# Optimization experiments

Measured on AMD Instinct MI355X. Metric: run time of the kernel, lower is better.

Reference implementation:

```python
import jax, jax.numpy as jnp
import numpy as np

B, S, HID = 2, 2048, 2048
NH, HD = 16, 128
EPS = 1e-5
ROPE_BASE = 10000.0


def setup_inputs() -> dict:
    key = jax.random.key(0)
    k1, k2, k3 = jax.random.split(key, 3)
    std = 1.0 / np.sqrt(HID)
    x = jax.random.normal(k1, (B, S, HID), jnp.float32)
    w_in = jax.random.truncated_normal(k2, -3.0, 3.0, (3 * NH * HD, HID), jnp.float32) * std
    std_o = std / np.sqrt(2.0)  # layer_id = 0 -> std / sqrt(2*(0+1))
    w_out = jax.random.truncated_normal(k3, -3.0, 3.0, (HID, NH * HD), jnp.float32) * std_o
    q_norm_w = jnp.ones((NH * HD,), jnp.float32)
    k_norm_w = jnp.ones((NH * HD,), jnp.float32)
    return {"x": x, "w_in": w_in, "w_out": w_out, "q_norm_w": q_norm_w, "k_norm_w": k_norm_w}


def _rms_norm(x, w, eps=EPS):
    ms = jnp.mean(x * x, axis=-1, keepdims=True)
    return x * jax.lax.rsqrt(ms + eps) * w


def _rope(x, offset=0):
    # x: [B, S, NH, HD]; rotate-half convention
    half = HD // 2
    inv_freq = 1.0 / (ROPE_BASE ** (jnp.arange(half, dtype=jnp.float32) / half))
    pos = jnp.arange(x.shape[1], dtype=jnp.float32) + offset
    ang = pos[:, None] * inv_freq                      # [S, half]
    cos = jnp.cos(ang)[None, :, None, :]
    sin = jnp.sin(ang)[None, :, None, :]
    x1, x2 = jnp.split(x, 2, axis=-1)
    return jnp.concatenate([x1 * cos - x2 * sin, x2 * cos + x1 * sin], axis=-1)


def reference(x, w_in, w_out, q_norm_w, k_norm_w):
    b, s, _ = x.shape
    qkv = jnp.einsum('bsh,oh->bso', x, w_in)           # [B, S, 3*NH*HD]
    q, k, v = jnp.split(qkv, 3, axis=-1)
    # qk-norm over the flat (NH*HD) axis, as in the torch module
    q = _rms_norm(q, q_norm_w)
    k = _rms_norm(k, k_norm_w)
    q = q.reshape(b, s, NH, HD)
    k = k.reshape(b, s, NH, HD)
    v = v.reshape(b, s, NH, HD)
    q = _rope(q)
    k = _rope(k)
    scale = 1.0 / np.sqrt(HD)
    scores = jnp.einsum('bqhd,bkhd->bhqk', q, k) * scale
    causal = jnp.tril(jnp.ones((s, s), dtype=bool))
    scores = jnp.where(causal[None, None, :, :], scores, jnp.finfo(scores.dtype).min)
    probs = jax.nn.softmax(scores, axis=-1)
    out = jnp.einsum('bhqk,bkhd->bqhd', probs, v).reshape(b, s, NH * HD)
    return jnp.einsum('bso,ho->bsh', out, w_out)
```

## Files before the change

### kernel.cpp

```cpp
#include <hip/hip_runtime.h>
#include <hip/hip_bf16.h>
#include <math.h>

#define B_   2
#define S_   2048
#define HID_ 2048
#define NH_  16
#define HD_  128
#define QKV_ (3 * NH_ * HD_)
#define EPS_ 1e-5f

typedef __bf16 bf16x8 __attribute__((ext_vector_type(8)));
typedef __bf16 bf16x4 __attribute__((ext_vector_type(4)));
typedef __bf16 bf16x2 __attribute__((ext_vector_type(2)));
typedef float  f32x4  __attribute__((ext_vector_type(4)));

__global__ __launch_bounds__(256) void cast3_f32_bf16(
    const float* __restrict__ a, __bf16* __restrict__ ao, int na4,
    const float* __restrict__ b, __bf16* __restrict__ bo, int nb4,
    const float* __restrict__ c, __bf16* __restrict__ co, int nc4) {
    int j = blockIdx.x * 256 + threadIdx.x;
    const float* src;
    __bf16* dst;
    if (j < na4) {
        src = a; dst = ao;
    } else {
        j -= na4;
        if (j < nb4) {
            src = b; dst = bo;
        } else {
            j -= nb4;
            if (j >= nc4) return;
            src = c; dst = co;
        }
    }
    float4 v = reinterpret_cast<const float4*>(src)[j];
    bf16x4 o = {(__bf16)v.x, (__bf16)v.y, (__bf16)v.z, (__bf16)v.w};
    reinterpret_cast<bf16x4*>(dst)[j] = o;
}

__device__ __forceinline__ void gload_lds16(const __bf16* g, __bf16* l) {
    __builtin_amdgcn_global_load_lds(
        (const __attribute__((address_space(1))) void*)g,
        (__attribute__((address_space(3))) void*)l, 16, 0, 0);
}

#define BARR  __builtin_amdgcn_s_barrier()
#define LGKM0 asm volatile("s_waitcnt lgkmcnt(0)" ::: "memory")
#define FENCE asm volatile("" ::: "memory")

__device__ __forceinline__ void read_a4x(const __bf16* bc, int wm, int lrow,
                                         int quad, int swz, int qq,
                                         bf16x8 (&af)[2][2]) {
#pragma unroll
    for (int i2 = 0; i2 < 2; ++i2)
#pragma unroll
        for (int kk = 0; kk < 2; ++kk)
            af[i2][kk] = *reinterpret_cast<const bf16x8*>(
                &bc[(wm * 128 + (qq * 2 + i2) * 16 + lrow) * 64 +
                    (((kk * 4 + quad) ^ swz) << 3)]);
}

__device__ __forceinline__ void read_b6(const __bf16* bc, int wn, int lrow,
                                        int quad, int swz,
                                        bf16x8 (&bf)[3][2]) {
#pragma unroll
    for (int j = 0; j < 3; ++j)
#pragma unroll
        for (int kk = 0; kk < 2; ++kk)
            bf[j][kk] = *reinterpret_cast<const bf16x8*>(
                &bc[16384 + (wn * 48 + j * 16 + lrow) * 64 +
                    (((kk * 4 + quad) ^ swz) << 3)]);
}

__device__ __forceinline__ void mfma12(int qq, const bf16x8 (&af)[2][2],
                                       const bf16x8 (&bf)[3][2],
                                       f32x4 (&acc)[8][3]) {
    __builtin_amdgcn_s_setprio(1);
#pragma unroll
    for (int i2 = 0; i2 < 2; ++i2)
#pragma unroll
        for (int j = 0; j < 3; ++j)
#pragma unroll
            for (int kk = 0; kk < 2; ++kk)
                acc[qq * 2 + i2][j] = __builtin_amdgcn_mfma_f32_16x16x32_bf16(
                    af[i2][kk], bf[j][kk], acc[qq * 2 + i2][j], 0, 0, 0);
    __builtin_amdgcn_s_setprio(0);
}

__global__ __launch_bounds__(512, 2) void gemm1_192(
    const __bf16* __restrict__ A, const __bf16* __restrict__ Bm,
    __bf16* __restrict__ C, int M, int N, int K) {
    __shared__ __bf16 lds[2][28672];

    const int tid  = threadIdx.x;
    const int w    = tid >> 6;
    const int lane = tid & 63;
    const int lrow = lane & 15;
    const int quad = lane >> 4;
    const int wm   = w >> 2;
    const int wn   = w & 3;
    const int swz  = lrow & 7;

    const int chunk = (int)gridDim.x >> 3;
    const int flat  = (int)blockIdx.x;
    const int vid   = (flat & 7) * chunk + (flat >> 3);
    const int m0 = (vid & 15) * 256;
    const int n0 = (vid >> 4) * 192;

    const int lr = lane >> 3;
    const int lg = lane & 7;
    const size_t K64 = (size_t)K * 64;
    const __bf16* pA = A  + (size_t)(m0 + w * 8 + lr) * K + ((lg ^ lr) << 3);
    const __bf16* pB = Bm + (size_t)(n0 + w * 8 + lr) * K + ((lg ^ lr) << 3);

#define STA(c, tt, dst) gload_lds16(pA + (size_t)(c) * K64 + (size_t)(tt) * 64, \
                                    (dst) + (c) * 4096 + w * 512)
#define STB(c, tt, dst) gload_lds16(pB + (size_t)(c) * K64 + (size_t)(tt) * 64, \
                                    (dst) + 16384 + (c) * 4096 + w * 512)

    f32x4 acc[8][3] = {};
    bf16x8 af[2][2], bf[3][2];

    {
        __bf16* d = &lds[0][0];
        STB(0, 0, d); STB(1, 0, d); STB(2, 0, d);
        FENCE;
        STA(0, 0, d); STA(2, 0, d);
        FENCE;
        STA(1, 0, d); STA(3, 0, d);
    }
    asm volatile("s_waitcnt vmcnt(2)" ::: "memory");
    BARR;

    const int nt = K >> 6;
    for (int t = 0; t < nt - 1; ++t) {
        __bf16* bc = &lds[t & 1][0];
        __bf16* bn = &lds[(t & 1) ^ 1][0];
        const int tn = t + 1;
        read_a4x(bc, wm, lrow, quad, swz, 0, af);
        read_b6(bc, wn, lrow, quad, swz, bf);
        STB(0, tn, bn); STB(1, tn, bn);
        BARR; LGKM0;
        mfma12(0, af, bf, acc);
        BARR;
        read_a4x(bc, wm, lrow, quad, swz, 1, af);
        STB(2, tn, bn);
        BARR; LGKM0;
        mfma12(1, af, bf, acc);
        asm volatile("s_waitcnt vmcnt(3)" ::: "memory");
        BARR;
        read_a4x(bc, wm, lrow, quad, swz, 2, af);
        STA(0, tn, bn); STA(2, tn, bn);
        BARR; LGKM0;
        mfma12(2, af, bf, acc);
        BARR;
        read_a4x(bc, wm, lrow, quad, swz, 3, af);
        STA(1, tn, bn); STA(3, tn, bn);
        BARR; LGKM0;
        mfma12(3, af, bf, acc);
        asm volatile("s_waitcnt vmcnt(2)" ::: "memory");
        BARR;
    }
    {
        __bf16* bc = &lds[(nt - 1) & 1][0];
        read_a4x(bc, wm, lrow, quad, swz, 0, af);
        read_b6(bc, wn, lrow, quad, swz, bf);
        BARR; LGKM0;
        mfma12(0, af, bf, acc);
        BARR;
        read_a4x(bc, wm, lrow, quad, swz, 1, af);
        BARR; LGKM0;
        mfma12(1, af, bf, acc);
        asm volatile("s_waitcnt vmcnt(0)" ::: "memory");
        BARR;
        read_a4x(bc, wm, lrow, quad, swz, 2, af);
        BARR; LGKM0;
        mfma12(2, af, bf, acc);
        BARR;
        read_a4x(bc, wm, lrow, quad, swz, 3, af);
        BARR; LGKM0;
        mfma12(3, af, bf, acc);
    }
#undef STA
#undef STB

#pragma unroll
    for (int mf = 0; mf < 8; ++mf) {
#pragma unroll
        for (int r = 0; r < 4; ++r) {
            int row = m0 + wm * 128 + mf * 16 + quad * 4 + r;
            size_t cb = (size_t)row * N + n0 + wn * 48 + lrow;
#pragma unroll
            for (int j = 0; j < 3; ++j)
                C[cb + j * 16] = (__bf16)acc[mf][j][r];
        }
    }
}

__device__ __forceinline__ void stage_tile6(
    const __bf16* pA, const __bf16* pB, __bf16* buf, int w, int K) {
#pragma unroll
    for (int s = 0; s < 2; ++s)
        gload_lds16(pA + (size_t)s * 64 * K, buf + s * 4096 + w * 512);
#pragma unroll
    for (int s = 0; s < 4; ++s)
        gload_lds16(pB + (size_t)s * 64 * K, buf + 8192 + s * 4096 + w * 512);
}

template <typename OutT>
__global__ __launch_bounds__(512, 2) void gemm_bt_8ph(
    const __bf16* __restrict__ A, const __bf16* __restrict__ Bm,
    OutT* __restrict__ C, int M, int N, int K) {
    __shared__ __bf16 lds[3][24576];

    const int tid  = threadIdx.x;
    const int w    = tid >> 6;
    const int lane = tid & 63;
    const int lrow = lane & 15;
    const int quad = lane >> 4;
    const int wm   = w >> 2;
    const int wn   = w & 3;

    const int chunk = (int)gridDim.x >> 3;
    const int flat  = (int)blockIdx.x;
    const int vid   = (flat & 7) * chunk + (flat >> 3);
    const int by    = vid & 31;
    const int bx    = vid >> 5;
    const int m0 = by * 128;
    const int n0 = bx * 256;

    const int lr = lane >> 3;
    const int lg = lane & 7;
    const __bf16* pA = A  + (size_t)(m0 + w * 8 + lr) * K + ((lg ^ lr) << 3);
    const __bf16* pB = Bm + (size_t)(n0 + w * 8 + lr) * K + ((lg ^ lr) << 3);

    const int nt = K >> 6;
    f32x4 acc[4][4] = {};

    stage_tile6(pA, pB, &lds[0][0], w, K);
    stage_tile6(pA + 64, pB + 64, &lds[1][0], w, K);

    int cur = 0;
    for (int t = 0; t < nt; ++t) {
        __bf16* bufc = &lds[cur][0];
        int nxt = cur + 2; if (nxt >= 3) nxt -= 3;
        if (t + 2 < nt) {
            stage_tile6(pA + (size_t)(t + 2) * 64, pB + (size_t)(t + 2) * 64,
                        &lds[nxt][0], w, K);
            asm volatile("s_waitcnt vmcnt(12)" ::: "memory");
        } else if (t + 1 < nt) {
            asm volatile("s_waitcnt vmcnt(6)" ::: "memory");
        } else {
            asm volatile("s_waitcnt vmcnt(0)" ::: "memory");
        }
        BARR;
        FENCE;

#pragma unroll
        for (int q = 0; q < 2; ++q) {
            bf16x8 af[2][2], bfv[4][2];
#pragma unroll
            for (int i = 0; i < 2; ++i)
#pragma unroll
                for (int kk = 0; kk < 2; ++kk)
                    af[i][kk] = *reinterpret_cast<const bf16x8*>(
                        &bufc[(wm * 64 + (q * 2 + i) * 16 + lrow) * 64 +
                              (((kk * 4 + quad) ^ (lrow & 7)) << 3)]);
#pragma unroll
            for (int j = 0; j < 4; ++j)
#pragma unroll
                for (int kk = 0; kk < 2; ++kk)
                    bfv[j][kk] = *reinterpret_cast<const bf16x8*>(
                        &bufc[8192 + (wn * 64 + j * 16 + lrow) * 64 +
                              (((kk * 4 + quad) ^ (lrow & 7)) << 3)]);
            BARR;
            FENCE;
            __builtin_amdgcn_s_setprio(1);
#pragma unroll
            for (int i = 0; i < 2; ++i)
#pragma unroll
                for (int j = 0; j < 4; ++j)
#pragma unroll
                    for (int kk = 0; kk < 2; ++kk)
                        acc[q * 2 + i][j] =
                            __builtin_amdgcn_mfma_f32_16x16x32_bf16(
                                af[i][kk], bfv[j][kk], acc[q * 2 + i][j],
                                0, 0, 0);
            __builtin_amdgcn_s_setprio(0);
        }
        BARR;
        FENCE;
        cur = (cur == 2) ? 0 : cur + 1;
    }

#pragma unroll
    for (int mi = 0; mi < 4; ++mi) {
#pragma unroll
        for (int r = 0; r < 4; ++r) {
            int row = m0 + wm * 64 + mi * 16 + quad * 4 + r;
            size_t basec = (size_t)row * N + n0 + wn * 64 + lrow;
#pragma unroll
            for (int nj = 0; nj < 4; ++nj)
                C[basec + nj * 16] = (OutT)acc[mi][nj][r];
        }
    }
}

__global__ __launch_bounds__(256) void normrope_kernel(
    __bf16* __restrict__ qkv, const float* __restrict__ qw,
    const float* __restrict__ kw) {
    const int row = blockIdx.x;
    const int sel = blockIdx.y;
    const int pos = row & (S_ - 1);
    __bf16* p = qkv + (size_t)row * QKV_ + sel * 2048;
    const float* w = sel ? kw : qw;

    __shared__ float buf[2048];
    __shared__ float red[4];
    const int tid = threadIdx.x;
    const int e   = tid * 8;

    bf16x8 t = *reinterpret_cast<const bf16x8*>(&p[e]);
    float xs[8];
    float ss = 0.f;
#pragma unroll
    for (int u = 0; u < 8; ++u) {
        xs[u] = (float)t[u];
        buf[e + u] = xs[u];
        ss += xs[u] * xs[u];
    }
#pragma unroll
    for (int off = 32; off > 0; off >>= 1) ss += __shfl_xor(ss, off, 64);
    if ((tid & 63) == 0) red[tid >> 6] = ss;
    __syncthreads();
    float total = red[0] + red[1] + red[2] + red[3];
    float scale = rsqrtf(total * (1.f / 2048.f) + EPS_);

    const float kfreq2 = -0.20762050593046f;
    const int jbase = e & 63;
    const bool first = (e & 127) < 64;
    const int ep = e ^ 64;

    float ps[8], ws[8], pw[8];
#pragma unroll
    for (int u = 0; u < 8; ++u) ps[u] = buf[ep + u];
    float4 w0 = *reinterpret_cast<const float4*>(&w[e]);
    float4 w1 = *reinterpret_cast<const float4*>(&w[e + 4]);
    float4 p0 = *reinterpret_cast<const float4*>(&w[ep]);
    float4 p1 = *reinterpret_cast<const float4*>(&w[ep + 4]);
    ws[0]=w0.x; ws[1]=w0.y; ws[2]=w0.z; ws[3]=w0.w;
    ws[4]=w1.x; ws[5]=w1.y; ws[6]=w1.z; ws[7]=w1.w;
    pw[0]=p0.x; pw[1]=p0.y; pw[2]=p0.z; pw[3]=p0.w;
    pw[4]=p1.x; pw[5]=p1.y; pw[6]=p1.z; pw[7]=p1.w;

    bf16x8 o8;
#pragma unroll
    for (int u = 0; u < 8; ++u) {
        float inv_freq = exp2f((float)(jbase + u) * kfreq2);
        float ang = (float)pos * inv_freq;
        float sn = __sinf(ang);
        float cs = __cosf(ang);
        float a  = xs[u] * scale * ws[u];
        float bb = ps[u] * scale * pw[u];
        float o  = first ? (a * cs - bb * sn) : (a * cs + bb * sn);
        o8[u] = (__bf16)o;
    }
    *reinterpret_cast<bf16x8*>(&p[e]) = o8;
}

#define VTP 36

__global__ __launch_bounds__(512, 4) void attn_mfma(
    const __bf16* __restrict__ qkv, __bf16* __restrict__ aout) {
    const int flat = (int)blockIdx.x;
    const int vid  = (flat & 7) * 64 + (flat >> 3);
    const int bh   = vid >> 4;
    const int qt   = 15 - (vid & 15);
    const int b    = bh >> 4;
    const int h    = bh & (NH_ - 1);
    const int q0   = qt * 128;
    const int tid  = threadIdx.x;
    const int w    = tid >> 6;
    const int lane = tid & 63;
    const int lrow = lane & 15;
    const int quad = lane >> 4;

    __shared__ __bf16 Ks[2][4][32 * 32];
    __shared__ __bf16 Vt[2][128 * VTP];
    __shared__ __bf16 Pb[8][16 * VTP];

    const size_t base = (size_t)(b * S_) * QKV_ + (size_t)h * HD_;
    const int qrow = q0 + w * 16 + lrow;

    bf16x8 qf[4];
#pragma unroll
    for (int kc = 0; kc < 4; ++kc)
        qf[kc] = *reinterpret_cast<const bf16x8*>(
            &qkv[base + (size_t)qrow * QKV_ + kc * 32 + quad * 8]);

    f32x4 o[8] = {};
    float lpart = 0.f;

    const int ktmax_w   = 4 * qt + (w >> 1);
    const int ktmax_blk = 4 * qt + 3;
    const float sl2 = 0.12751743671f;

    const __bf16* kg0 = qkv + base + 2048 +
                        (size_t)((w & 1) * 16 + (lane >> 2)) * QKV_ +
                        (w >> 1) * 32 + (lane & 3) * 8;
    const int g  = tid >> 4;
    const int kp = tid & 15;
    const __bf16* vg0 = qkv + base + 4096 + (size_t)(kp * 2) * QKV_ + g * 8;

    gload_lds16(kg0, &Ks[0][w >> 1][(w & 1) * 512]);
    bf16x8 v0 = {}, v1 = {};
    if (tid < 256) {
        v0 = *reinterpret_cast<const bf16x8*>(vg0);
        v1 = *reinterpret_cast<const bf16x8*>(vg0 + QKV_);
    }

    for (int kt = 0; kt <= ktmax_blk; ++kt) {
        const int buf = kt & 1;
        if (tid < 256) {
#pragma unroll
            for (int u = 0; u < 8; ++u) {
                bf16x2 pr = {v0[u], v1[u]};
                *reinterpret_cast<bf16x2*>(
                    &Vt[buf][(g * 8 + u) * VTP + kp * 2]) = pr;
            }
        }
        __syncthreads();
        if (kt < ktmax_blk) {
            const __bf16* kg = kg0 + (size_t)(kt + 1) * 32 * QKV_;
            gload_lds16(kg, &Ks[buf ^ 1][w >> 1][(w & 1) * 512]);
            if (tid < 256) {
                const __bf16* vg = vg0 + (size_t)(kt + 1) * 32 * QKV_;
                v0 = *reinterpret_cast<const bf16x8*>(vg);
                v1 = *reinterpret_cast<const bf16x8*>(vg + QKV_);
            }
        }
        if (kt <= ktmax_w) {
            f32x4 sc[2] = {};
            __builtin_amdgcn_s_setprio(1);
#pragma unroll
            for (int kc = 0; kc < 4; ++kc) {
                bf16x8 kf0 = *reinterpret_cast<const bf16x8*>(
                    &Ks[buf][kc][lrow * 32 + quad * 8]);
                bf16x8 kf1 = *reinterpret_cast<const bf16x8*>(
                    &Ks[buf][kc][(16 + lrow) * 32 + quad * 8]);
                sc[0] = __builtin_amdgcn_mfma_f32_16x16x32_bf16(
                    kf0, qf[kc], sc[0], 0, 0, 0);
                sc[1] = __builtin_amdgcn_mfma_f32_16x16x32_bf16(
                    kf1, qf[kc], sc[1], 0, 0, 0);
            }
            __builtin_amdgcn_s_setprio(0);
            const bool diag = (kt == ktmax_w);
            float p[2][4];
#pragma unroll
            for (int m2 = 0; m2 < 2; ++m2)
#pragma unroll
                for (int r = 0; r < 4; ++r) {
                    float s = sc[m2][r] * sl2 - 32.f;
                    if (diag && kt * 32 + m2 * 16 + quad * 4 + r > qrow)
                        s = -1e30f;
                    p[m2][r] = exp2f(s);
                    lpart += p[m2][r];
                }
#pragma unroll
            for (int m2 = 0; m2 < 2; ++m2) {
                bf16x4 pb = {(__bf16)p[m2][0], (__bf16)p[m2][1],
                             (__bf16)p[m2][2], (__bf16)p[m2][3]};
                *reinterpret_cast<bf16x4*>(
                    &Pb[w][lrow * VTP + m2 * 16 + quad * 4]) = pb;
            }
            bf16x8 pf = *reinterpret_cast<const bf16x8*>(
                &Pb[w][lrow * VTP + quad * 8]);
            __builtin_amdgcn_s_setprio(1);
#pragma unroll
            for (int dt = 0; dt < 8; ++dt) {
                bf16x8 vf = *reinterpret_cast<const bf16x8*>(
                    &Vt[buf][(dt * 16 + lrow) * VTP + quad * 8]);
                o[dt] = __builtin_amdgcn_mfma_f32_16x16x32_bf16(
                    vf, pf, o[dt], 0, 0, 0);
            }
            __builtin_amdgcn_s_setprio(0);
        }
    }

    lpart += __shfl_xor(lpart, 16, 64);
    lpart += __shfl_xor(lpart, 32, 64);
    const float invl = 1.f / lpart;
    const size_t orow = (size_t)(b * S_ + qrow) * (NH_ * HD_) + (size_t)h * HD_;
#pragma unroll
    for (int dt = 0; dt < 8; ++dt) {
        bf16x4 ov = {(__bf16)(o[dt][0] * invl), (__bf16)(o[dt][1] * invl),
                     (__bf16)(o[dt][2] * invl), (__bf16)(o[dt][3] * invl)};
        *reinterpret_cast<bf16x4*>(&aout[orow + dt * 16 + quad * 4]) = ov;
    }
}

extern "C" void kernel_launch(void* const* d_in, const int* in_sizes, int n_in,
                              void* d_out, int out_size, void* d_ws,
                              size_t ws_size, hipStream_t stream) {
    const float* x     = (const float*)d_in[0];
    const float* w_in  = (const float*)d_in[1];
    const float* w_out = (const float*)d_in[2];
    const float* qw    = (const float*)d_in[3];
    const float* kw    = (const float*)d_in[4];
    float* out = (float*)d_out;

    const int M = B_ * S_;
    char* ws = (char*)d_ws;
    __bf16* qkv_b   = (__bf16*)(ws);
    __bf16* w_out_b = (__bf16*)(ws + (size_t)50331648);
    __bf16* x_b     = (__bf16*)(ws + (size_t)58720256);
    __bf16* attn_b  = x_b;
    __bf16* w_in_b  = (__bf16*)(ws + (size_t)75497472);

    dim3 blk(256);

    {
        const int na4 = (M * HID_) / 4;
        const int nb4 = (QKV_ * HID_) / 4;
        const int nc4 = (HID_ * NH_ * HD_) / 4;
        const int tot = na4 + nb4 + nc4;
        cast3_f32_bf16<<<dim3((tot + 255) / 256), blk, 0, stream>>>(
            x, x_b, na4, w_in, w_in_b, nb4, w_out, w_out_b, nc4);
    }

    gemm1_192<<<dim3((M / 256) * (QKV_ / 192)), dim3(512), 0, stream>>>(
        x_b, w_in_b, qkv_b, M, QKV_, HID_);
    normrope_kernel<<<dim3(M, 2), blk, 0, stream>>>(qkv_b, qw, kw);
    attn_mfma<<<dim3((S_ / 128) * B_ * NH_), dim3(512), 0, stream>>>(
        qkv_b, attn_b);
    gemm_bt_8ph<float><<<dim3((M / 128) * (HID_ / 256)), dim3(512), 0,
                         stream>>>(attn_b, w_out_b, out, M, HID_, NH_ * HD_);
}
```

Before: 392.8 us.

## Pair high and low causal query tiles per attention block and swizzle K LDS

Each attention block now processes two query tiles (qt = 8+p and 7-p) that share the same K/V stream, which balances causal work across blocks and reuses each loaded K/V tile for two query tiles. The grid halves to 256 blocks and launch bounds drop to 2 blocks per SM, since registers double for two accumulator sets. An XOR swizzle is added to the K tile LDS layout to reduce bank conflicts on fragment reads. The risks are lower occupancy, higher register pressure and fewer blocks to spread across compute units.

Result: slower. 490.3 us (+24.8%).

```diff
diff --git a/kernel.cpp b/kernel.cpp
--- a/kernel.cpp
+++ b/kernel.cpp
@@ -371,15 +371,66 @@
 
 #define VTP 36
 
-__global__ __launch_bounds__(512, 4) void attn_mfma(
+__device__ __forceinline__ void attn_tile_step(
+    const __bf16* KsB, const __bf16* VtB, __bf16* PbW,
+    int kt, int ktw, int lrow, int quad, int kgq,
+    const bf16x8 (&qf)[4], int qrow, f32x4 (&o)[8], float& lp) {
+    if (kt > ktw) return;
+    const float sl2 = 0.12751743671f;
+    f32x4 sc[2] = {};
+    __builtin_amdgcn_s_setprio(1);
+#pragma unroll
+    for (int kc = 0; kc < 4; ++kc) {
+        bf16x8 kf0 = *reinterpret_cast<const bf16x8*>(
+            &KsB[kc * 1024 + lrow * 32 + kgq]);
+        bf16x8 kf1 = *reinterpret_cast<const bf16x8*>(
+            &KsB[kc * 1024 + (16 + lrow) * 32 + kgq]);
+        sc[0] = __builtin_amdgcn_mfma_f32_16x16x32_bf16(
+            kf0, qf[kc], sc[0], 0, 0, 0);
+        sc[1] = __builtin_amdgcn_mfma_f32_16x16x32_bf16(
+            kf1, qf[kc], sc[1], 0, 0, 0);
+    }
+    __builtin_amdgcn_s_setprio(0);
+    const bool diag = (kt == ktw);
+    float p[2][4];
+#pragma unroll
+    for (int m2 = 0; m2 < 2; ++m2)
+#pragma unroll
+        for (int r = 0; r < 4; ++r) {
+            float s = sc[m2][r] * sl2 - 32.f;
+            if (diag && kt * 32 + m2 * 16 + quad * 4 + r > qrow)
+                s = -1e30f;
+            p[m2][r] = exp2f(s);
+            lp += p[m2][r];
+        }
+#pragma unroll
+    for (int m2 = 0; m2 < 2; ++m2) {
+        bf16x4 pb = {(__bf16)p[m2][0], (__bf16)p[m2][1],
+                     (__bf16)p[m2][2], (__bf16)p[m2][3]};
+        *reinterpret_cast<bf16x4*>(&PbW[lrow * VTP + m2 * 16 + quad * 4]) = pb;
+    }
+    bf16x8 pf = *reinterpret_cast<const bf16x8*>(&PbW[lrow * VTP + quad * 8]);
+    __builtin_amdgcn_s_setprio(1);
+#pragma unroll
+    for (int dt = 0; dt < 8; ++dt) {
+        bf16x8 vf = *reinterpret_cast<const bf16x8*>(
+            &VtB[(dt * 16 + lrow) * VTP + quad * 8]);
+        o[dt] = __builtin_amdgcn_mfma_f32_16x16x32_bf16(
+            vf, pf, o[dt], 0, 0, 0);
+    }
+    __builtin_amdgcn_s_setprio(0);
+}
+
+__global__ __launch_bounds__(512, 2) void attn_mfma(
     const __bf16* __restrict__ qkv, __bf16* __restrict__ aout) {
     const int flat = (int)blockIdx.x;
-    const int vid  = (flat & 7) * 64 + (flat >> 3);
-    const int bh   = vid >> 4;
-    const int qt   = 15 - (vid & 15);
+    const int vid  = (flat & 7) * 32 + (flat >> 3);
+    const int bh   = vid >> 3;
+    const int pr   = vid & 7;
+    const int qtH  = 8 + pr;
+    const int qtL  = 7 - pr;
     const int b    = bh >> 4;
     const int h    = bh & (NH_ - 1);
-    const int q0   = qt * 128;
     const int tid  = threadIdx.x;
     const int w    = tid >> 6;
     const int lane = tid & 63;
@@ -391,24 +442,29 @@
     __shared__ __bf16 Pb[8][16 * VTP];
 
     const size_t base = (size_t)(b * S_) * QKV_ + (size_t)h * HD_;
-    const int qrow = q0 + w * 16 + lrow;
-
-    bf16x8 qf[4];
-#pragma unroll
-    for (int kc = 0; kc < 4; ++kc)
-        qf[kc] = *reinterpret_cast<const bf16x8*>(
-            &qkv[base + (size_t)qrow * QKV_ + kc * 32 + quad * 8]);
-
-    f32x4 o[8] = {};
-    float lpart = 0.f;
-
-    const int ktmax_w   = 4 * qt + (w >> 1);
-    const int ktmax_blk = 4 * qt + 3;
-    const float sl2 = 0.12751743671f;
+    const int qrowH = qtH * 128 + w * 16 + lrow;
+    const int qrowL = qtL * 128 + w * 16 + lrow;
+
+    bf16x8 qfH[4], qfL[4];
+#pragma unroll
+    for (int kc = 0; kc < 4; ++kc) {
+        qfH[kc] = *reinterpret_cast<const bf16x8*>(
+            &qkv[base + (size_t)qrowH * QKV_ + kc * 32 + quad * 8]);
+        qfL[kc] = *reinterpret_cast<const bf16x8*>(
+            &qkv[base + (size_t)qrowL * QKV_ + kc * 32 + quad * 8]);
+    }
+
+    f32x4 oH[8] = {}, oL[8] = {};
+    float lpH = 0.f, lpL = 0.f;
+
+    const int ktmaxH_w  = 4 * qtH + (w >> 1);
+    const int ktmaxL_w  = 4 * qtL + (w >> 1);
+    const int ktmax_blk = 4 * qtH + 3;
+    const int kgq = (quad ^ ((lrow >> 1) & 3)) * 8;
 
     const __bf16* kg0 = qkv + base + 2048 +
                         (size_t)((w & 1) * 16 + (lane >> 2)) * QKV_ +
-                        (w >> 1) * 32 + (lane & 3) * 8;
+                        (w >> 1) * 32 + (((lane & 3) ^ ((lane >> 3) & 3)) << 3);
     const int g  = tid >> 4;
     const int kp = tid & 15;
     const __bf16* vg0 = qkv + base + 4096 + (size_t)(kp * 2) * QKV_ + g * 8;
@@ -425,9 +481,9 @@
         if (tid < 256) {
 #pragma unroll
             for (int u = 0; u < 8; ++u) {
-                bf16x2 pr = {v0[u], v1[u]};
+                bf16x2 pr2 = {v0[u], v1[u]};
                 *reinterpret_cast<bf16x2*>(
-                    &Vt[buf][(g * 8 + u) * VTP + kp * 2]) = pr;
+                    &Vt[buf][(g * 8 + u) * VTP + kp * 2]) = pr2;
             }
         }
         __syncthreads();
@@ -440,63 +496,28 @@
                 v1 = *reinterpret_cast<const bf16x8*>(vg + QKV_);
             }
         }
-        if (kt <= ktmax_w) {
-            f32x4 sc[2] = {};
-            __builtin_amdgcn_s_setprio(1);
-#pragma unroll
-            for (int kc = 0; kc < 4; ++kc) {
-                bf16x8 kf0 = *reinterpret_cast<const bf16x8*>(
-                    &Ks[buf][kc][lrow * 32 + quad * 8]);
-                bf16x8 kf1 = *reinterpret_cast<const bf16x8*>(
-                    &Ks[buf][kc][(16 + lrow) * 32 + quad * 8]);
-                sc[0] = __builtin_amdgcn_mfma_f32_16x16x32_bf16(
-                    kf0, qf[kc], sc[0], 0, 0, 0);
-                sc[1] = __builtin_amdgcn_mfma_f32_16x16x32_bf16(
-                    kf1, qf[kc], sc[1], 0, 0, 0);
-            }
-            __builtin_amdgcn_s_setprio(0);
-            const bool diag = (kt == ktmax_w);
-            float p[2][4];
-#pragma unroll
-            for (int m2 = 0; m2 < 2; ++m2)
-#pragma unroll
-                for (int r = 0; r < 4; ++r) {
-                    float s = sc[m2][r] * sl2 - 32.f;
-                    if (diag && kt * 32 + m2 * 16 + quad * 4 + r > qrow)
-                        s = -1e30f;
-                    p[m2][r] = exp2f(s);
-                    lpart += p[m2][r];
-                }
-#pragma unroll
-            for (int m2 = 0; m2 < 2; ++m2) {
-                bf16x4 pb = {(__bf16)p[m2][0], (__bf16)p[m2][1],
-                             (__bf16)p[m2][2], (__bf16)p[m2][3]};
-                *reinterpret_cast<bf16x4*>(
-                    &Pb[w][lrow * VTP + m2 * 16 + quad * 4]) = pb;
-            }
-            bf16x8 pf = *reinterpret_cast<const bf16x8*>(
-                &Pb[w][lrow * VTP + quad * 8]);
-            __builtin_amdgcn_s_setprio(1);
-#pragma unroll
-            for (int dt = 0; dt < 8; ++dt) {
-                bf16x8 vf = *reinterpret_cast<const bf16x8*>(
-                    &Vt[buf][(dt * 16 + lrow) * VTP + quad * 8]);
-                o[dt] = __builtin_amdgcn_mfma_f32_16x16x32_bf16(
-                    vf, pf, o[dt], 0, 0, 0);
-            }
-            __builtin_amdgcn_s_setprio(0);
-        }
-    }
-
-    lpart += __shfl_xor(lpart, 16, 64);
-    lpart += __shfl_xor(lpart, 32, 64);
-    const float invl = 1.f / lpart;
-    const size_t orow = (size_t)(b * S_ + qrow) * (NH_ * HD_) + (size_t)h * HD_;
-#pragma unroll
-    for (int dt = 0; dt < 8; ++dt) {
-        bf16x4 ov = {(__bf16)(o[dt][0] * invl), (__bf16)(o[dt][1] * invl),
-                     (__bf16)(o[dt][2] * invl), (__bf16)(o[dt][3] * invl)};
-        *reinterpret_cast<bf16x4*>(&aout[orow + dt * 16 + quad * 4]) = ov;
+        attn_tile_step(&Ks[buf][0][0], &Vt[buf][0], &Pb[w][0],
+                       kt, ktmaxH_w, lrow, quad, kgq, qfH, qrowH, oH, lpH);
+        attn_tile_step(&Ks[buf][0][0], &Vt[buf][0], &Pb[w][0],
+                       kt, ktmaxL_w, lrow, quad, kgq, qfL, qrowL, oL, lpL);
+    }
+
+#pragma unroll
+    for (int sel = 0; sel < 2; ++sel) {
+        f32x4* o = sel ? oL : oH;
+        float lp = sel ? lpL : lpH;
+        const int qrow = sel ? qrowL : qrowH;
+        lp += __shfl_xor(lp, 16, 64);
+        lp += __shfl_xor(lp, 32, 64);
+        const float invl = 1.f / lp;
+        const size_t orow =
+            (size_t)(b * S_ + qrow) * (NH_ * HD_) + (size_t)h * HD_;
+#pragma unroll
+        for (int dt = 0; dt < 8; ++dt) {
+            bf16x4 ov = {(__bf16)(o[dt][0] * invl), (__bf16)(o[dt][1] * invl),
+                         (__bf16)(o[dt][2] * invl), (__bf16)(o[dt][3] * invl)};
+            *reinterpret_cast<bf16x4*>(&aout[orow + dt * 16 + quad * 4]) = ov;
+        }
     }
 }
 
@@ -532,8 +553,7 @@
     gemm1_192<<<dim3((M / 256) * (QKV_ / 192)), dim3(512), 0, stream>>>(
         x_b, w_in_b, qkv_b, M, QKV_, HID_);
     normrope_kernel<<<dim3(M, 2), blk, 0, stream>>>(qkv_b, qw, kw);
-    attn_mfma<<<dim3((S_ / 128) * B_ * NH_), dim3(512), 0, stream>>>(
-        qkv_b, attn_b);
+    attn_mfma<<<dim3(256), dim3(512), 0, stream>>>(qkv_b, attn_b);
     gemm_bt_8ph<float><<<dim3((M / 128) * (HID_ / 256)), dim3(512), 0,
                          stream>>>(attn_b, w_out_b, out, M, HID_, NH_ * HD_);
 }
```
